# Performance work log

Hardware: AMD Instinct MI355X
Metric: run time of the kernel (lower is better)

## Reference

```python
import jax, jax.numpy as jnp
import numpy as np

B, S, J, D = 64, 2048, 25, 3
FEAT_DIM = 128
COMPUTED = 12  # pos(3) + vel(3) + acc(3) + angles(3)
IN_MLP = COMPUTED * J  # 300
HID = FEAT_DIM * 2     # 256
CONN = np.array([(0, 1), (1, 5), (1, 6), (5, 7), (7, 9), (6, 8), (8, 10),
                 (1, 11), (1, 12), (11, 13), (13, 15), (12, 14), (14, 16)], dtype=np.int32)


def setup_inputs() -> dict:
    key = jax.random.key(0)
    ks = jax.random.split(key, 8)
    return {
        "poses": jax.random.normal(ks[0], (B, S, J, D), dtype=jnp.float32),
        "W1": jax.random.normal(ks[1], (IN_MLP, HID), dtype=jnp.float32) * 0.05,
        "b1": jnp.zeros((HID,), jnp.float32),
        "gamma": jnp.ones((HID,), jnp.float32),
        "beta": jnp.zeros((HID,), jnp.float32),
        "running_mean": jnp.zeros((HID,), jnp.float32),
        "running_var": jnp.ones((HID,), jnp.float32),
        "W2": jax.random.normal(ks[2], (HID, FEAT_DIM), dtype=jnp.float32) * 0.05,
        "b2": jnp.zeros((FEAT_DIM,), jnp.float32),
        "joint_weights": jnp.ones((J,), jnp.float32),
    }


def reference(poses, W1, b1, gamma, beta, running_mean, running_var, W2, b2, joint_weights):
    b, s, j, d = poses.shape
    # --- root-centering + max-distance normalization ---
    p = poses - poses[:, :, 0:1, :]
    dist = jnp.linalg.norm(p, axis=-1, keepdims=True)           # [B,S,J,1]
    max_dist = jnp.max(dist, axis=2, keepdims=True)             # [B,S,1,1]
    p = p / (max_dist + 1e-8)
    # --- velocity / acceleration (zero-padded first frames) ---
    zpad = jnp.zeros_like(p[:, :1])
    vel = jnp.concatenate([zpad, p[:, 1:] - p[:, :-1]], axis=1)
    acc = jnp.concatenate([zpad, vel[:, 1:] - vel[:, :-1]], axis=1)
    # --- joint angles: vectorized gather + normalize + acos (replaces B*S*13 python loop) ---
    v1 = p[:, :, CONN[:, 1], :] - p[:, :, CONN[:, 0], :]        # [B,S,13,3]
    vnorm = jnp.maximum(jnp.linalg.norm(v1, axis=-1, keepdims=True), 1e-12)  # F.normalize eps
    ang = jnp.arccos(jnp.clip(v1 / vnorm, -1.0, 1.0))           # [B,S,13,3]
    ang = ang.reshape(b, s, -1)                                 # [B,S,39]
    pad = jnp.zeros((b, s, j * 3 - ang.shape[-1]), ang.dtype)   # pad to J*3=75
    angles = jnp.concatenate([ang, pad], axis=-1).reshape(b, s, j, 3)
    # --- combine, weight, project ---
    feat = jnp.concatenate([p, vel, acc, angles], axis=-1)      # [B,S,J,12]
    feat = feat * joint_weights.reshape(1, 1, j, 1)
    x = feat.reshape(b * s, -1)                                 # [B*S,300]
    x = x @ W1 + b1
    x = gamma * (x - running_mean) / jnp.sqrt(running_var + 1e-5) + beta  # BN eval mode
    x = jax.nn.relu(x)                                          # dropout = identity (eval)
    x = x @ W2 + b2
    return x.reshape(b, s, -1)                                  # [B,S,128]
```

## Files before the change

### kernel.cpp

```cpp
#include <hip/hip_runtime.h>
#include <stdint.h>


#define S_    2048
#define MT_   64
#define TPB   512
#define HID_  256
#define OUT_  128
#define NTOK  131072

typedef __attribute__((ext_vector_type(8))) _Float16 half8;
typedef __attribute__((ext_vector_type(4))) float    floatx4;

#define C0M 0x0ECDB118675110ULL
#define C1M 0x0FDECBA9786540ULL

__device__ __forceinline__ float facos(float x) {
    float ax = fabsf(x);
    float p = fmaf(ax, -0.0187293f, 0.0742610f);
    p = fmaf(ax, p, -0.2121144f);
    p = fmaf(ax, p, 1.5707288f);
    float r = __builtin_amdgcn_sqrtf(1.f - ax) * p;
    return x < 0.f ? 3.14159265358979f - r : r;
}

__global__ void prep_kernel(const float* __restrict__ W1, const float* __restrict__ b1,
                            const float* __restrict__ gamma, const float* __restrict__ beta,
                            const float* __restrict__ rmean, const float* __restrict__ rvar,
                            const float* __restrict__ W2, const float* __restrict__ jw,
                            _Float16* __restrict__ w1p,
                            _Float16* __restrict__ w2p,
                            float* __restrict__ b1p) {
    int idx = blockIdx.x * 256 + threadIdx.x;
    if (idx < 352 * 256) {
        int k = idx >> 8, n = idx & 255;
        float a = gamma[n] * __builtin_amdgcn_rsqf(rvar[n] + 1e-5f);
        float v = 0.f;
        if (k < 288) {
            int d = k / 96, loc = k - d * 96;
            if (loc < 75) {
                int j = loc / 3, c = loc - j * 3;
                const float* Wb = W1 + (j * 12 + c) * HID_ + n;
                float wp = Wb[0], wv = Wb[3 * HID_], wa = Wb[6 * HID_];
                float t = (d == 0) ? (wp + wv + wa) : (d == 1 ? -(wv + 2.f * wa) : wa);
                v = t * a * jw[j];
            }
        } else {
            int q = k - 288;
            if (q < 39) {
                int e = q / 3, aa = q - e * 3;
                v = W1[(e * 12 + 9 + aa) * HID_ + n] * a * jw[e];
            }
        }
        int blk = (k >> 5) * 16 + (n >> 4);
        int off = blk * 512 + (((k >> 3) & 3) * 16 + (n & 15)) * 8 + (k & 7);
        w1p[off] = (_Float16)v;
    } else if (idx < 352 * 256 + 256 * 128) {
        int i2 = idx - 352 * 256;
        int k = i2 >> 7, n = i2 & 127;
        int blk = (k >> 5) * 8 + (n >> 4);
        int off = blk * 512 + (((k >> 3) & 3) * 16 + (n & 15)) * 8 + (k & 7);
        w2p[off] = (_Float16)W2[k * OUT_ + n];
    } else if (idx < 352 * 256 + 256 * 128 + 256) {
        int n = idx - (352 * 256 + 256 * 128);
        float a = gamma[n] * __builtin_amdgcn_rsqf(rvar[n] + 1e-5f);
        b1p[n] = fmaf(a, b1[n] - rmean[n], beta[n]);
    }
}

#define L_CCB 0
#define L_AB  13728
#define L_RAW 22944
#define L_RS  43424
#define L_TOT 44480

__global__ __launch_bounds__(TPB, 6) void pose_mlp(
    const float* __restrict__ poses,
    const _Float16* __restrict__ w1p,
    const _Float16* __restrict__ w2p,
    const float* __restrict__ b1p,
    const float* __restrict__ b2,
    float* __restrict__ out)
{
    __shared__ __align__(16) unsigned char smem[L_TOT];
    const int tid  = threadIdx.x;
    const int lane = tid & 63;
    const int wv   = tid >> 6;
    const int t0   = blockIdx.x * MT_;
    const int s0   = t0 & (S_ - 1);

    _Float16* ccb = (_Float16*)(smem + L_CCB);
    _Float16* ab  = (_Float16*)(smem + L_AB);
    float*    raw = (float*)(smem + L_RAW);
    float4*   rs  = (float4*)(smem + L_RS);

    half8 bw[2];
    #pragma unroll
    for (int ni = 0; ni < 2; ni++)
        bw[ni] = *(const half8*)(w1p + (unsigned)(wv * 2 + ni) * 512 + lane * 8);

    #pragma unroll
    for (int it = 0; it < 10; it++) {
        int i = it * TPB + tid;
        int src = t0 * 75 - 150 + i;
        if (s0 == 0) { if (i < 75) src += 150; else if (i < 150) src += 75; }
        src = src < NTOK * 75 - 1 ? src : NTOK * 75 - 1;
        raw[i] = poses[src];
    }
    __syncthreads();

    if (tid < 132) {
        int f = tid >> 1, h = tid & 1;
        const float* R = raw + f * 75;
        float r0 = R[0], r1 = R[1], r2 = R[2];
        float m2 = 0.f;
        #pragma unroll
        for (int jj = 0; jj < 13; jj++) {
            int j = h * 13 + jj;
            if (j < 25) {
                float dx = R[j * 3]     - r0;
                float dy = R[j * 3 + 1] - r1;
                float dz = R[j * 3 + 2] - r2;
                m2 = fmaxf(m2, fmaf(dx, dx, fmaf(dy, dy, dz * dz)));
            }
        }
        m2 = fmaxf(m2, __shfl_xor(m2, 1));
        if (h == 0) {
            float sc = __builtin_amdgcn_rcpf(__builtin_amdgcn_sqrtf(m2) + 1e-8f);
            rs[f] = make_float4(r0, r1, r2, sc);
        }
    }
    __syncthreads();

    #pragma unroll 1
    for (int i = tid; i < 66 * 32; i += TPB) {
        int f = i >> 5, j = i & 31;
        _Float16* C = ccb + f * 104;
        if (j < 25) {
            const float* R = raw + f * 75 + j * 3;
            float4 q = rs[f];
            C[j * 3 + 0] = (_Float16)((R[0] - q.x) * q.w);
            C[j * 3 + 1] = (_Float16)((R[1] - q.y) * q.w);
            C[j * 3 + 2] = (_Float16)((R[2] - q.z) * q.w);
        } else {
            int c = 75 + (j - 25) * 3;
            C[c] = (_Float16)0.f; C[c + 1] = (_Float16)0.f; C[c + 2] = (_Float16)0.f;
        }
    }

    #pragma unroll 1
    for (int i = tid; i < 64 * 16; i += TPB) {
        int tt = i >> 4, e = i & 15;
        _Float16* A = ab + tt * 72;
        if (e < 13) {
            const float* R = raw + (tt + 2) * 75;
            int a0 = (int)((C0M >> (4 * e)) & 15) * 3;
            int a1 = (((int)((C1M >> (4 * e)) & 15)) + 1) * 3;
            float vx = R[a1] - R[a0], vy = R[a1 + 1] - R[a0 + 1], vz = R[a1 + 2] - R[a0 + 2];
            float d  = fmaf(vx, vx, fmaf(vy, vy, vz * vz));
            float inv = __builtin_amdgcn_rcpf(fmaxf(__builtin_amdgcn_sqrtf(d), 1e-12f));
            A[e * 3 + 0] = (_Float16)facos(fminf(fmaxf(vx * inv, -1.f), 1.f));
            A[e * 3 + 1] = (_Float16)facos(fminf(fmaxf(vy * inv, -1.f), 1.f));
            A[e * 3 + 2] = (_Float16)facos(fminf(fmaxf(vz * inv, -1.f), 1.f));
        } else {
            int c0 = 39 + (e - 13);
            #pragma unroll
            for (int k = 0; k < 9; k++) { int c = c0 + 3 * k; if (c < 64) A[c] = (_Float16)0.f; }
        }
    }
    __syncthreads();

    floatx4 acc[4][2];
    #pragma unroll
    for (int mi = 0; mi < 4; mi++)
        #pragma unroll
        for (int ni = 0; ni < 2; ni++) acc[mi][ni] = (floatx4){0.f, 0.f, 0.f, 0.f};

    unsigned rowb[4];
    #pragma unroll
    for (int mi = 0; mi < 4; mi++)
        rowb[mi] = (unsigned)(mi * 16 + (lane & 15) + 2) * 104 + (lane >> 4) * 8;

    int ko = 0, fofs = 0;
    #pragma unroll 1
    for (int kc = 0; kc < 9; kc++) {
        half8 bn[2];
        #pragma unroll
        for (int ni = 0; ni < 2; ni++)
            bn[ni] = *(const half8*)(w1p + (unsigned)((kc + 1) * 16 + wv * 2 + ni) * 512 + lane * 8);
        half8 af[4];
        #pragma unroll
        for (int mi = 0; mi < 4; mi++)
            af[mi] = *(const half8*)(ccb + rowb[mi] + ko - fofs);
        #pragma unroll
        for (int mi = 0; mi < 4; mi++)
            #pragma unroll
            for (int ni = 0; ni < 2; ni++)
                acc[mi][ni] = __builtin_amdgcn_mfma_f32_16x16x32_f16(
                    af[mi], bw[ni], acc[mi][ni], 0, 0, 0);
        bw[0] = bn[0]; bw[1] = bn[1];
        ko += 32; if (ko == 96) { ko = 0; fofs += 104; }
    }
    {
        unsigned rowa[4];
        #pragma unroll
        for (int mi = 0; mi < 4; mi++)
            rowa[mi] = (unsigned)(mi * 16 + (lane & 15)) * 72 + (lane >> 4) * 8;
        #pragma unroll
        for (int kc = 9; kc < 11; kc++) {
            half8 bn[2];
            if (kc < 10) {
                #pragma unroll
                for (int ni = 0; ni < 2; ni++)
                    bn[ni] = *(const half8*)(w1p + (unsigned)((kc + 1) * 16 + wv * 2 + ni) * 512 + lane * 8);
            }
            half8 af[4];
            #pragma unroll
            for (int mi = 0; mi < 4; mi++)
                af[mi] = *(const half8*)(ab + rowa[mi] + (kc - 9) * 32);
            #pragma unroll
            for (int mi = 0; mi < 4; mi++)
                #pragma unroll
                for (int ni = 0; ni < 2; ni++)
                    acc[mi][ni] = __builtin_amdgcn_mfma_f32_16x16x32_f16(
                        af[mi], bw[ni], acc[mi][ni], 0, 0, 0);
            if (kc < 10) { bw[0] = bn[0]; bw[1] = bn[1]; }
        }
    }

    half8 bw2 = *(const half8*)(w2p + (unsigned)wv * 512 + lane * 8);

    __syncthreads();

    _Float16* hid = (_Float16*)smem;
    float bv[2];
    #pragma unroll
    for (int ni = 0; ni < 2; ni++) bv[ni] = b1p[wv * 32 + ni * 16 + (lane & 15)];
    #pragma unroll
    for (int mi = 0; mi < 4; mi++)
        #pragma unroll
        for (int ni = 0; ni < 2; ni++)
            #pragma unroll
            for (int r = 0; r < 4; r++) {
                float v = fmaxf(acc[mi][ni][r] + bv[ni], 0.f);
                int m   = mi * 16 + (lane >> 4) * 4 + r;
                int col = wv * 32 + ni * 16 + (lane & 15);
                hid[m * 264 + col] = (_Float16)v;
            }
    __syncthreads();

    floatx4 acc2[4];
    #pragma unroll
    for (int mi = 0; mi < 4; mi++) acc2[mi] = (floatx4){0.f, 0.f, 0.f, 0.f};

    #pragma unroll 1
    for (int kc = 0; kc < 8; kc++) {
        half8 bn2;
        if (kc < 7)
            bn2 = *(const half8*)(w2p + (unsigned)((kc + 1) * 8 + wv) * 512 + lane * 8);
        half8 af[4];
        #pragma unroll
        for (int mi = 0; mi < 4; mi++)
            af[mi] = *(const half8*)(hid + (mi * 16 + (lane & 15)) * 264 + kc * 32 + (lane >> 4) * 8);
        #pragma unroll
        for (int mi = 0; mi < 4; mi++)
            acc2[mi] = __builtin_amdgcn_mfma_f32_16x16x32_f16(
                af[mi], bw2, acc2[mi], 0, 0, 0);
        if (kc < 7) bw2 = bn2;
    }

    float c2 = b2[wv * 16 + (lane & 15)];
    #pragma unroll
    for (int mi = 0; mi < 4; mi++)
        #pragma unroll
        for (int r = 0; r < 4; r++) {
            int m   = mi * 16 + (lane >> 4) * 4 + r;
            int col = wv * 16 + (lane & 15);
            out[(size_t)(t0 + m) * OUT_ + col] = acc2[mi][r] + c2;
        }
}

extern "C" void kernel_launch(void* const* d_in, const int* in_sizes, int n_in,
                              void* d_out, int out_size, void* d_ws, size_t ws_size,
                              hipStream_t stream) {
    (void)in_sizes; (void)n_in; (void)out_size; (void)ws_size;
    const float* poses = (const float*)d_in[0];
    const float* W1    = (const float*)d_in[1];
    const float* b1    = (const float*)d_in[2];
    const float* gamma = (const float*)d_in[3];
    const float* beta  = (const float*)d_in[4];
    const float* rmean = (const float*)d_in[5];
    const float* rvar  = (const float*)d_in[6];
    const float* W2    = (const float*)d_in[7];
    const float* b2    = (const float*)d_in[8];
    const float* jw    = (const float*)d_in[9];

    _Float16* w1p = (_Float16*)d_ws;
    _Float16* w2p = w1p + 352 * HID_;
    float* b1p = (float*)((char*)d_ws + (352 * HID_ + HID_ * OUT_) * 2);

    prep_kernel<<<481, 256, 0, stream>>>(W1, b1, gamma, beta, rmean, rvar, W2, jw,
                                         w1p, w2p, b1p);
    pose_mlp<<<2048, TPB, 0, stream>>>(poses, w1p, w2p, b1p, b2, (float*)d_out);
}
```

Measured before the change: 146.5 us.

## Halve token tile to 32, compact LDS layout, stage output for vector nontemporal stores

Cuts tokens per block from 64 to 32 and doubles the grid. LDS row strides are compacted (88/40 halves) so per-block shared memory drops and launch bounds rise to 8 blocks per CU. The epilogue now stages outputs through LDS and writes them with coalesced float4 nontemporal stores instead of scattered scalar stores. In exchange, W1/W2 fragment loads are amortised over fewer rows, and the two-frame halo reload grows relative to useful work.

```diff
diff --git a/kernel.cpp b/kernel.cpp
--- a/kernel.cpp
+++ b/kernel.cpp
@@ -3,14 +3,16 @@
 
 
 #define S_    2048
-#define MT_   64
+#define MT_   32
 #define TPB   512
 #define HID_  256
 #define OUT_  128
 #define NTOK  131072
+#define F_    34
 
 typedef __attribute__((ext_vector_type(8))) _Float16 half8;
 typedef __attribute__((ext_vector_type(4))) float    floatx4;
+typedef __attribute__((ext_vector_type(4))) float    f4_t;
 
 #define C0M 0x0ECDB118675110ULL
 #define C1M 0x0FDECBA9786540ULL
@@ -69,12 +71,12 @@
 }
 
 #define L_CCB 0
-#define L_AB  13728
-#define L_RAW 22944
-#define L_RS  43424
-#define L_TOT 44480
-
-__global__ __launch_bounds__(TPB, 6) void pose_mlp(
+#define L_AB  6000
+#define L_RAW 8608
+#define L_RS  18816
+#define L_TOT 19360
+
+__global__ __launch_bounds__(TPB, 8) void pose_mlp(
     const float* __restrict__ poses,
     const _Float16* __restrict__ w1p,
     const _Float16* __restrict__ w2p,
@@ -100,16 +102,21 @@
         bw[ni] = *(const half8*)(w1p + (unsigned)(wv * 2 + ni) * 512 + lane * 8);
 
     #pragma unroll
-    for (int it = 0; it < 10; it++) {
+    for (int it = 0; it < 5; it++) {
         int i = it * TPB + tid;
-        int src = t0 * 75 - 150 + i;
-        if (s0 == 0) { if (i < 75) src += 150; else if (i < 150) src += 75; }
-        src = src < NTOK * 75 - 1 ? src : NTOK * 75 - 1;
-        raw[i] = poses[src];
-    }
-    __syncthreads();
-
-    if (tid < 132) {
+        if (i < F_ * 75) {
+            int src = t0 * 75 - 150 + i;
+            if (s0 == 0) { if (i < 75) src += 150; else if (i < 150) src += 75; }
+            raw[i] = poses[src];
+        }
+    }
+    if (tid < 32) {
+        if (tid < 8) ccb[F_ * 88 + tid] = (_Float16)0.f;
+        else         ab[MT_ * 40 + (tid - 8)] = (_Float16)0.f;
+    }
+    __syncthreads();
+
+    if (tid < F_ * 2) {
         int f = tid >> 1, h = tid & 1;
         const float* R = raw + f * 75;
         float r0 = R[0], r1 = R[1], r2 = R[2];
@@ -133,9 +140,9 @@
     __syncthreads();
 
     #pragma unroll 1
-    for (int i = tid; i < 66 * 32; i += TPB) {
+    for (int i = tid; i < F_ * 32; i += TPB) {
         int f = i >> 5, j = i & 31;
-        _Float16* C = ccb + f * 104;
+        _Float16* C = ccb + f * 88;
         if (j < 25) {
             const float* R = raw + f * 75 + j * 3;
             float4 q = rs[f];
@@ -143,15 +150,15 @@
             C[j * 3 + 1] = (_Float16)((R[1] - q.y) * q.w);
             C[j * 3 + 2] = (_Float16)((R[2] - q.z) * q.w);
         } else {
-            int c = 75 + (j - 25) * 3;
-            C[c] = (_Float16)0.f; C[c + 1] = (_Float16)0.f; C[c + 2] = (_Float16)0.f;
-        }
-    }
-
-    #pragma unroll 1
-    for (int i = tid; i < 64 * 16; i += TPB) {
-        int tt = i >> 4, e = i & 15;
-        _Float16* A = ab + tt * 72;
+            int c = 75 + (j - 25) * 2;
+            C[c] = (_Float16)0.f;
+            if (c + 1 < 88) C[c + 1] = (_Float16)0.f;
+        }
+    }
+
+    {
+        int tt = tid >> 4, e = tid & 15;
+        _Float16* A = ab + tt * 40;
         if (e < 13) {
             const float* R = raw + (tt + 2) * 75;
             int a0 = (int)((C0M >> (4 * e)) & 15) * 3;
@@ -162,50 +169,48 @@
             A[e * 3 + 0] = (_Float16)facos(fminf(fmaxf(vx * inv, -1.f), 1.f));
             A[e * 3 + 1] = (_Float16)facos(fminf(fmaxf(vy * inv, -1.f), 1.f));
             A[e * 3 + 2] = (_Float16)facos(fminf(fmaxf(vz * inv, -1.f), 1.f));
-        } else {
-            int c0 = 39 + (e - 13);
-            #pragma unroll
-            for (int k = 0; k < 9; k++) { int c = c0 + 3 * k; if (c < 64) A[c] = (_Float16)0.f; }
-        }
-    }
-    __syncthreads();
-
-    floatx4 acc[4][2];
-    #pragma unroll
-    for (int mi = 0; mi < 4; mi++)
+        } else if (e == 13) {
+            A[39] = (_Float16)0.f;
+        }
+    }
+    __syncthreads();
+
+    floatx4 acc[2][2];
+    #pragma unroll
+    for (int mi = 0; mi < 2; mi++)
         #pragma unroll
         for (int ni = 0; ni < 2; ni++) acc[mi][ni] = (floatx4){0.f, 0.f, 0.f, 0.f};
 
-    unsigned rowb[4];
-    #pragma unroll
-    for (int mi = 0; mi < 4; mi++)
-        rowb[mi] = (unsigned)(mi * 16 + (lane & 15) + 2) * 104 + (lane >> 4) * 8;
-
-    int ko = 0, fofs = 0;
+    int rowb[2];
+    #pragma unroll
+    for (int mi = 0; mi < 2; mi++)
+        rowb[mi] = (mi * 16 + (lane & 15) + 2) * 88 + (lane >> 4) * 8;
+
+    int koff = 0;
     #pragma unroll 1
     for (int kc = 0; kc < 9; kc++) {
         half8 bn[2];
         #pragma unroll
         for (int ni = 0; ni < 2; ni++)
             bn[ni] = *(const half8*)(w1p + (unsigned)((kc + 1) * 16 + wv * 2 + ni) * 512 + lane * 8);
-        half8 af[4];
-        #pragma unroll
-        for (int mi = 0; mi < 4; mi++)
-            af[mi] = *(const half8*)(ccb + rowb[mi] + ko - fofs);
-        #pragma unroll
-        for (int mi = 0; mi < 4; mi++)
+        half8 af[2];
+        #pragma unroll
+        for (int mi = 0; mi < 2; mi++)
+            af[mi] = *(const half8*)(ccb + rowb[mi] + koff);
+        #pragma unroll
+        for (int mi = 0; mi < 2; mi++)
             #pragma unroll
             for (int ni = 0; ni < 2; ni++)
                 acc[mi][ni] = __builtin_amdgcn_mfma_f32_16x16x32_f16(
                     af[mi], bw[ni], acc[mi][ni], 0, 0, 0);
         bw[0] = bn[0]; bw[1] = bn[1];
-        ko += 32; if (ko == 96) { ko = 0; fofs += 104; }
+        koff += 32; if (kc == 2 || kc == 5) koff -= 184;
     }
     {
-        unsigned rowa[4];
-        #pragma unroll
-        for (int mi = 0; mi < 4; mi++)
-            rowa[mi] = (unsigned)(mi * 16 + (lane & 15)) * 72 + (lane >> 4) * 8;
+        int rowa[2];
+        #pragma unroll
+        for (int mi = 0; mi < 2; mi++)
+            rowa[mi] = (mi * 16 + (lane & 15)) * 40 + (lane >> 4) * 8;
         #pragma unroll
         for (int kc = 9; kc < 11; kc++) {
             half8 bn[2];
@@ -214,12 +219,12 @@
                 for (int ni = 0; ni < 2; ni++)
                     bn[ni] = *(const half8*)(w1p + (unsigned)((kc + 1) * 16 + wv * 2 + ni) * 512 + lane * 8);
             }
-            half8 af[4];
+            half8 af[2];
             #pragma unroll
-            for (int mi = 0; mi < 4; mi++)
+            for (int mi = 0; mi < 2; mi++)
                 af[mi] = *(const half8*)(ab + rowa[mi] + (kc - 9) * 32);
             #pragma unroll
-            for (int mi = 0; mi < 4; mi++)
+            for (int mi = 0; mi < 2; mi++)
                 #pragma unroll
                 for (int ni = 0; ni < 2; ni++)
                     acc[mi][ni] = __builtin_amdgcn_mfma_f32_16x16x32_f16(
@@ -237,7 +242,7 @@
     #pragma unroll
     for (int ni = 0; ni < 2; ni++) bv[ni] = b1p[wv * 32 + ni * 16 + (lane & 15)];
     #pragma unroll
-    for (int mi = 0; mi < 4; mi++)
+    for (int mi = 0; mi < 2; mi++)
         #pragma unroll
         for (int ni = 0; ni < 2; ni++)
             #pragma unroll
@@ -249,35 +254,45 @@
             }
     __syncthreads();
 
-    floatx4 acc2[4];
-    #pragma unroll
-    for (int mi = 0; mi < 4; mi++) acc2[mi] = (floatx4){0.f, 0.f, 0.f, 0.f};
+    floatx4 acc2[2];
+    #pragma unroll
+    for (int mi = 0; mi < 2; mi++) acc2[mi] = (floatx4){0.f, 0.f, 0.f, 0.f};
 
     #pragma unroll 1
     for (int kc = 0; kc < 8; kc++) {
         half8 bn2;
         if (kc < 7)
             bn2 = *(const half8*)(w2p + (unsigned)((kc + 1) * 8 + wv) * 512 + lane * 8);
-        half8 af[4];
-        #pragma unroll
-        for (int mi = 0; mi < 4; mi++)
+        half8 af[2];
+        #pragma unroll
+        for (int mi = 0; mi < 2; mi++)
             af[mi] = *(const half8*)(hid + (mi * 16 + (lane & 15)) * 264 + kc * 32 + (lane >> 4) * 8);
         #pragma unroll
-        for (int mi = 0; mi < 4; mi++)
+        for (int mi = 0; mi < 2; mi++)
             acc2[mi] = __builtin_amdgcn_mfma_f32_16x16x32_f16(
                 af[mi], bw2, acc2[mi], 0, 0, 0);
         if (kc < 7) bw2 = bn2;
     }
 
     float c2 = b2[wv * 16 + (lane & 15)];
-    #pragma unroll
-    for (int mi = 0; mi < 4; mi++)
+    __syncthreads();
+
+    float* obuf = (float*)smem;
+    #pragma unroll
+    for (int mi = 0; mi < 2; mi++)
         #pragma unroll
         for (int r = 0; r < 4; r++) {
-            int m   = mi * 16 + (lane >> 4) * 4 + r;
-            int col = wv * 16 + (lane & 15);
-            out[(size_t)(t0 + m) * OUT_ + col] = acc2[mi][r] + c2;
-        }
+            int m = mi * 16 + (lane >> 4) * 4 + r;
+            obuf[m * 132 + wv * 16 + (lane & 15)] = acc2[mi][r] + c2;
+        }
+    __syncthreads();
+    #pragma unroll
+    for (int k = 0; k < 2; k++) {
+        int idx = k * TPB + tid;
+        int row = idx >> 5, c4 = idx & 31;
+        f4_t v = *(const f4_t*)(obuf + row * 132 + c4 * 4);
+        __builtin_nontemporal_store(v, (f4_t*)out + (size_t)t0 * 32 + idx);
+    }
 }
 
 extern "C" void kernel_launch(void* const* d_in, const int* in_sizes, int n_in,
@@ -301,5 +316,5 @@
 
     prep_kernel<<<481, 256, 0, stream>>>(W1, b1, gamma, beta, rmean, rvar, W2, jw,
                                          w1p, w2p, b1p);
-    pose_mlp<<<2048, TPB, 0, stream>>>(poses, w1p, w2p, b1p, b2, (float*)d_out);
+    pose_mlp<<<4096, TPB, 0, stream>>>(poses, w1p, w2p, b1p, b2, (float*)d_out);
 }
```

Result: slower. 154.7 us (+5.6%).

## Compact LDS layout, vectorize pose loads, stage output for coalesced nontemporal stores

Applied to the files above, without the earlier changes.

Shrinks the LDS tiles for positions and angles (row strides of 88 and 40 halves instead of 104 and 72), reducing the per-block footprint and the zero-fill work. Pose loads now use float2 vector reads after a small scalar head, and the angle computation is moved ahead of the max-distance pass, which is spread over four lanes per frame instead of two. The layer-1 and layer-2 biases are folded into the accumulator initialization. Output goes through LDS so it can be written as coalesced float4 nontemporal stores, at the cost of an extra barrier and LDS round trip.

```diff
diff --git a/kernel.cpp b/kernel.cpp
--- a/kernel.cpp
+++ b/kernel.cpp
@@ -8,9 +8,11 @@
 #define HID_  256
 #define OUT_  128
 #define NTOK  131072
+#define F_    66
 
 typedef __attribute__((ext_vector_type(8))) _Float16 half8;
 typedef __attribute__((ext_vector_type(4))) float    floatx4;
+typedef __attribute__((ext_vector_type(4))) float    f4_t;
 
 #define C0M 0x0ECDB118675110ULL
 #define C1M 0x0FDECBA9786540ULL
@@ -31,9 +33,9 @@
                             _Float16* __restrict__ w1p,
                             _Float16* __restrict__ w2p,
                             float* __restrict__ b1p) {
-    int idx = blockIdx.x * 256 + threadIdx.x;
-    if (idx < 352 * 256) {
-        int k = idx >> 8, n = idx & 255;
+    int bid = blockIdx.x, tid = threadIdx.x;
+    if (bid < 352) {
+        int k = bid, n = tid;
         float a = gamma[n] * __builtin_amdgcn_rsqf(rvar[n] + 1e-5f);
         float v = 0.f;
         if (k < 288) {
@@ -55,24 +57,24 @@
         int blk = (k >> 5) * 16 + (n >> 4);
         int off = blk * 512 + (((k >> 3) & 3) * 16 + (n & 15)) * 8 + (k & 7);
         w1p[off] = (_Float16)v;
-    } else if (idx < 352 * 256 + 256 * 128) {
-        int i2 = idx - 352 * 256;
+    } else if (bid < 480) {
+        int i2 = (bid - 352) * 256 + tid;
         int k = i2 >> 7, n = i2 & 127;
         int blk = (k >> 5) * 8 + (n >> 4);
         int off = blk * 512 + (((k >> 3) & 3) * 16 + (n & 15)) * 8 + (k & 7);
         w2p[off] = (_Float16)W2[k * OUT_ + n];
-    } else if (idx < 352 * 256 + 256 * 128 + 256) {
-        int n = idx - (352 * 256 + 256 * 128);
+    } else {
+        int n = tid;
         float a = gamma[n] * __builtin_amdgcn_rsqf(rvar[n] + 1e-5f);
         b1p[n] = fmaf(a, b1[n] - rmean[n], beta[n]);
     }
 }
 
 #define L_CCB 0
-#define L_AB  13728
-#define L_RAW 22944
-#define L_RS  43424
-#define L_TOT 44480
+#define L_AB  11632
+#define L_RAW 16800
+#define L_RS  36608
+#define L_TOT 37696
 
 __global__ __launch_bounds__(TPB, 6) void pose_mlp(
     const float* __restrict__ poses,
@@ -98,25 +100,56 @@
     #pragma unroll
     for (int ni = 0; ni < 2; ni++)
         bw[ni] = *(const half8*)(w1p + (unsigned)(wv * 2 + ni) * 512 + lane * 8);
-
-    #pragma unroll
-    for (int it = 0; it < 10; it++) {
-        int i = it * TPB + tid;
-        int src = t0 * 75 - 150 + i;
-        if (s0 == 0) { if (i < 75) src += 150; else if (i < 150) src += 75; }
-        src = src < NTOK * 75 - 1 ? src : NTOK * 75 - 1;
-        raw[i] = poses[src];
-    }
-    __syncthreads();
-
-    if (tid < 132) {
-        int f = tid >> 1, h = tid & 1;
+    float bv[2];
+    #pragma unroll
+    for (int ni = 0; ni < 2; ni++) bv[ni] = b1p[wv * 32 + ni * 16 + (lane & 15)];
+    float c2 = b2[wv * 16 + (lane & 15)];
+
+    if (tid < 152) {
+        int src = t0 * 75 - 150 + tid;
+        if (s0 == 0) { if (tid < 75) src += 150; else if (tid < 150) src += 75; }
+        raw[tid] = poses[src];
+    }
+    {
+        const float2* ps = (const float2*)(poses + (size_t)t0 * 75 + 2);
+        #pragma unroll 1
+        for (int i = tid; i < 2399; i += TPB) {
+            float2 v = ps[i];
+            *(float2*)(raw + 152 + 2 * i) = v;
+        }
+    }
+    if (tid < 96) {
+        if (tid < 8)       ccb[F_ * 88 + tid] = (_Float16)0.f;
+        else if (tid < 32) ab[MT_ * 40 + (tid - 8)] = (_Float16)0.f;
+        else               ab[(tid - 32) * 40 + 39] = (_Float16)0.f;
+    }
+    __syncthreads();
+
+    #pragma unroll
+    for (int r2 = 0; r2 < 2; r2++) {
+        int i = r2 * TPB + tid;
+        int tt = i >> 4, e = i & 15;
+        if (e < 13) {
+            const float* R = raw + (tt + 2) * 75;
+            int a0 = (int)((C0M >> (4 * e)) & 15) * 3;
+            int a1 = (((int)((C1M >> (4 * e)) & 15)) + 1) * 3;
+            float vx = R[a1] - R[a0], vy = R[a1 + 1] - R[a0 + 1], vz = R[a1 + 2] - R[a0 + 2];
+            float d  = fmaf(vx, vx, fmaf(vy, vy, vz * vz));
+            float inv = __builtin_amdgcn_rcpf(fmaxf(__builtin_amdgcn_sqrtf(d), 1e-12f));
+            _Float16* A = ab + tt * 40;
+            A[e * 3 + 0] = (_Float16)facos(fminf(fmaxf(vx * inv, -1.f), 1.f));
+            A[e * 3 + 1] = (_Float16)facos(fminf(fmaxf(vy * inv, -1.f), 1.f));
+            A[e * 3 + 2] = (_Float16)facos(fminf(fmaxf(vz * inv, -1.f), 1.f));
+        }
+    }
+    if (tid < F_ * 4) {
+        int f = tid >> 2, q = tid & 3;
         const float* R = raw + f * 75;
         float r0 = R[0], r1 = R[1], r2 = R[2];
         float m2 = 0.f;
         #pragma unroll
-        for (int jj = 0; jj < 13; jj++) {
-            int j = h * 13 + jj;
+        for (int jj = 0; jj < 7; jj++) {
+            int j = q * 7 + jj;
             if (j < 25) {
                 float dx = R[j * 3]     - r0;
                 float dy = R[j * 3 + 1] - r1;
@@ -125,7 +158,8 @@
             }
         }
         m2 = fmaxf(m2, __shfl_xor(m2, 1));
-        if (h == 0) {
+        m2 = fmaxf(m2, __shfl_xor(m2, 2));
+        if (q == 0) {
             float sc = __builtin_amdgcn_rcpf(__builtin_amdgcn_sqrtf(m2) + 1e-8f);
             rs[f] = make_float4(r0, r1, r2, sc);
         }
@@ -133,9 +167,9 @@
     __syncthreads();
 
     #pragma unroll 1
-    for (int i = tid; i < 66 * 32; i += TPB) {
+    for (int i = tid; i < F_ * 32; i += TPB) {
         int f = i >> 5, j = i & 31;
-        _Float16* C = ccb + f * 104;
+        _Float16* C = ccb + f * 88;
         if (j < 25) {
             const float* R = raw + f * 75 + j * 3;
             float4 q = rs[f];
@@ -143,29 +177,9 @@
             C[j * 3 + 1] = (_Float16)((R[1] - q.y) * q.w);
             C[j * 3 + 2] = (_Float16)((R[2] - q.z) * q.w);
         } else {
-            int c = 75 + (j - 25) * 3;
-            C[c] = (_Float16)0.f; C[c + 1] = (_Float16)0.f; C[c + 2] = (_Float16)0.f;
-        }
-    }
-
-    #pragma unroll 1
-    for (int i = tid; i < 64 * 16; i += TPB) {
-        int tt = i >> 4, e = i & 15;
-        _Float16* A = ab + tt * 72;
-        if (e < 13) {
-            const float* R = raw + (tt + 2) * 75;
-            int a0 = (int)((C0M >> (4 * e)) & 15) * 3;
-            int a1 = (((int)((C1M >> (4 * e)) & 15)) + 1) * 3;
-            float vx = R[a1] - R[a0], vy = R[a1 + 1] - R[a0 + 1], vz = R[a1 + 2] - R[a0 + 2];
-            float d  = fmaf(vx, vx, fmaf(vy, vy, vz * vz));
-            float inv = __builtin_amdgcn_rcpf(fmaxf(__builtin_amdgcn_sqrtf(d), 1e-12f));
-            A[e * 3 + 0] = (_Float16)facos(fminf(fmaxf(vx * inv, -1.f), 1.f));
-            A[e * 3 + 1] = (_Float16)facos(fminf(fmaxf(vy * inv, -1.f), 1.f));
-            A[e * 3 + 2] = (_Float16)facos(fminf(fmaxf(vz * inv, -1.f), 1.f));
-        } else {
-            int c0 = 39 + (e - 13);
-            #pragma unroll
-            for (int k = 0; k < 9; k++) { int c = c0 + 3 * k; if (c < 64) A[c] = (_Float16)0.f; }
+            int c = 75 + (j - 25) * 2;
+            C[c] = (_Float16)0.f;
+            if (c + 1 < 88) C[c + 1] = (_Float16)0.f;
         }
     }
     __syncthreads();
@@ -174,14 +188,15 @@
     #pragma unroll
     for (int mi = 0; mi < 4; mi++)
         #pragma unroll
-        for (int ni = 0; ni < 2; ni++) acc[mi][ni] = (floatx4){0.f, 0.f, 0.f, 0.f};
-
-    unsigned rowb[4];
+        for (int ni = 0; ni < 2; ni++)
+            acc[mi][ni] = (floatx4){bv[ni], bv[ni], bv[ni], bv[ni]};
+
+    int rowb[4];
     #pragma unroll
     for (int mi = 0; mi < 4; mi++)
-        rowb[mi] = (unsigned)(mi * 16 + (lane & 15) + 2) * 104 + (lane >> 4) * 8;
-
-    int ko = 0, fofs = 0;
+        rowb[mi] = (mi * 16 + (lane & 15) + 2) * 88 + (lane >> 4) * 8;
+
+    int koff = 0;
     #pragma unroll 1
     for (int kc = 0; kc < 9; kc++) {
         half8 bn[2];
@@ -191,7 +206,7 @@
         half8 af[4];
         #pragma unroll
         for (int mi = 0; mi < 4; mi++)
-            af[mi] = *(const half8*)(ccb + rowb[mi] + ko - fofs);
+            af[mi] = *(const half8*)(ccb + rowb[mi] + koff);
         #pragma unroll
         for (int mi = 0; mi < 4; mi++)
             #pragma unroll
@@ -199,13 +214,13 @@
                 acc[mi][ni] = __builtin_amdgcn_mfma_f32_16x16x32_f16(
                     af[mi], bw[ni], acc[mi][ni], 0, 0, 0);
         bw[0] = bn[0]; bw[1] = bn[1];
-        ko += 32; if (ko == 96) { ko = 0; fofs += 104; }
+        koff += 32; if (kc == 2 || kc == 5) koff -= 184;
     }
     {
-        unsigned rowa[4];
-        #pragma unroll
-        for (int mi = 0; mi < 4; mi++)
-            rowa[mi] = (unsigned)(mi * 16 + (lane & 15)) * 72 + (lane >> 4) * 8;
+        int rowa[4];
+        #pragma unroll
+        for (int mi = 0; mi < 4; mi++)
+            rowa[mi] = (mi * 16 + (lane & 15)) * 40 + (lane >> 4) * 8;
         #pragma unroll
         for (int kc = 9; kc < 11; kc++) {
             half8 bn[2];
@@ -233,16 +248,13 @@
     __syncthreads();
 
     _Float16* hid = (_Float16*)smem;
-    float bv[2];
-    #pragma unroll
-    for (int ni = 0; ni < 2; ni++) bv[ni] = b1p[wv * 32 + ni * 16 + (lane & 15)];
     #pragma unroll
     for (int mi = 0; mi < 4; mi++)
         #pragma unroll
         for (int ni = 0; ni < 2; ni++)
             #pragma unroll
             for (int r = 0; r < 4; r++) {
-                float v = fmaxf(acc[mi][ni][r] + bv[ni], 0.f);
+                float v = fmaxf(acc[mi][ni][r], 0.f);
                 int m   = mi * 16 + (lane >> 4) * 4 + r;
                 int col = wv * 32 + ni * 16 + (lane & 15);
                 hid[m * 264 + col] = (_Float16)v;
@@ -251,7 +263,7 @@
 
     floatx4 acc2[4];
     #pragma unroll
-    for (int mi = 0; mi < 4; mi++) acc2[mi] = (floatx4){0.f, 0.f, 0.f, 0.f};
+    for (int mi = 0; mi < 4; mi++) acc2[mi] = (floatx4){c2, c2, c2, c2};
 
     #pragma unroll 1
     for (int kc = 0; kc < 8; kc++) {
@@ -268,16 +280,24 @@
                 af[mi], bw2, acc2[mi], 0, 0, 0);
         if (kc < 7) bw2 = bn2;
     }
-
-    float c2 = b2[wv * 16 + (lane & 15)];
+    __syncthreads();
+
+    float* obuf = (float*)smem;
     #pragma unroll
     for (int mi = 0; mi < 4; mi++)
         #pragma unroll
         for (int r = 0; r < 4; r++) {
-            int m   = mi * 16 + (lane >> 4) * 4 + r;
-            int col = wv * 16 + (lane & 15);
-            out[(size_t)(t0 + m) * OUT_ + col] = acc2[mi][r] + c2;
-        }
+            int m = mi * 16 + (lane >> 4) * 4 + r;
+            obuf[m * 132 + wv * 16 + (lane & 15)] = acc2[mi][r];
+        }
+    __syncthreads();
+    #pragma unroll
+    for (int k = 0; k < 4; k++) {
+        int idx = k * TPB + tid;
+        int row = idx >> 5, c4 = idx & 31;
+        f4_t v = *(const f4_t*)(obuf + row * 132 + c4 * 4);
+        __builtin_nontemporal_store(v, (f4_t*)out + (size_t)t0 * 32 + idx);
+    }
 }
 
 extern "C" void kernel_launch(void* const* d_in, const int* in_sizes, int n_in,
```

Result: slower. 162.8 us (+11.1%).
